# Kernel optimization log

Hardware: AMD Instinct MI355X
Metric: run time of the kernel (lower is better)

## Reference

```python
import jax, jax.numpy as jnp
import numpy as np

INPUT_DIM = 512
NUM_CLASSES = 1000


def setup_inputs() -> dict:
    key = jax.random.key(0)
    kx, kw, kb = jax.random.split(key, 3)
    x = jax.random.normal(kx, (16384, INPUT_DIM), dtype=jnp.float32)
    # Stacked per-class Linear(input_dim, 2) params: W [C, 2, D], b [C, 2]
    lim = 1.0 / np.sqrt(INPUT_DIM)
    W = jax.random.uniform(kw, (NUM_CLASSES, 2, INPUT_DIM), dtype=jnp.float32, minval=-lim, maxval=lim)
    b = jax.random.uniform(kb, (NUM_CLASSES, 2), dtype=jnp.float32, minval=-lim, maxval=lim)
    return {"x": x, "W": W, "b": b}


def reference(x, W, b):
    # logits[b, c, t] = x[b, :] @ W[c, t, :] + b[c, t]
    logits = jnp.einsum("bd,ctd->bct", x, W) + b[None, :, :]  # [B, C, 2]
    # LogSoftmax over the 2 logits per class (torch dim=1 of the [B,2] slice)
    return jax.nn.log_softmax(logits, axis=-1)
```

## Files before the change

### kernel.cpp

```cpp
#include <hip/hip_runtime.h>
#include <cstdint>
#include <cstddef>

typedef unsigned short u16;
typedef unsigned int u32;
typedef __bf16 bf16x8 __attribute__((ext_vector_type(8)));
typedef float f32x4 __attribute__((ext_vector_type(4)));
typedef float f32x2 __attribute__((ext_vector_type(2)));
typedef u32 u32x4 __attribute__((ext_vector_type(4)));

#define M_TOT 16384
#define C_TOT 1000
#define N_PAD 1024
#define K_TOT 512
#define OUT_STRIDE 2000
#define BM 128
#define BN 128
#define BK 32
#define NT 16
#define NWG 1024

__device__ __forceinline__ u16 f2bf(float f) {
  u32 u = __float_as_uint(f);
  u = (u + 0x7FFFu + ((u >> 16) & 1u)) >> 16;
  return (u16)u;
}

__device__ __forceinline__ u32 cvtpk(float lo, float hi) {
  u32 d;
  asm("v_cvt_pk_bf16_f32 %0, %1, %2" : "=v"(d) : "v"(lo), "v"(hi));
  return d;
}

__global__ __launch_bounds__(256) void wprep_kernel(const float* __restrict__ W,
                                                    const float* __restrict__ b,
                                                    u16* __restrict__ wd,
                                                    float* __restrict__ bd) {
  const int i = blockIdx.x * 256 + threadIdx.x;
  const int c = i >> 6;
  const int seg = i & 63;
  ushort4 r0 = {0, 0, 0, 0}, r1 = {0, 0, 0, 0};
  if (c < C_TOT) {
    const float4* w0 = (const float4*)(W + (size_t)(2 * c) * K_TOT) + seg * 2;
    const float4* w1 = (const float4*)(W + (size_t)(2 * c + 1) * K_TOT) + seg * 2;
    float4 a0 = w0[0], a1 = w0[1], c0 = w1[0], c1 = w1[1];
    r0.x = f2bf(a0.x - c0.x); r0.y = f2bf(a0.y - c0.y);
    r0.z = f2bf(a0.z - c0.z); r0.w = f2bf(a0.w - c0.w);
    r1.x = f2bf(a1.x - c1.x); r1.y = f2bf(a1.y - c1.y);
    r1.z = f2bf(a1.z - c1.z); r1.w = f2bf(a1.w - c1.w);
    if (seg == 0) bd[c] = b[2 * c] - b[2 * c + 1];
  } else if (seg == 0) {
    bd[c] = 0.0f;
  }
  ushort4* d = (ushort4*)(wd + (size_t)c * K_TOT);
  d[seg * 2] = r0;
  d[seg * 2 + 1] = r1;
}

__device__ __forceinline__ void gload_lds(const u16* g, u16* l) {
  __builtin_amdgcn_global_load_lds((const __attribute__((address_space(1))) u32*)g,
                                   (__attribute__((address_space(3))) u32*)l, 16, 0, 0);
}

__device__ __forceinline__ void stage8k(const u16* __restrict__ gbase,
                                        u16* lb, int tid) {
#pragma unroll
  for (int i = 0; i < 2; ++i) {
    const int g = i * 256 + tid;
    const int lrow = g >> 3;
    const int u = (g & 7) ^ (lrow & 7);
    const int r = lrow | ((u >> 2) << 6);
    const int q = u & 3;
    gload_lds(gbase + (size_t)r * K_TOT + q * 8, lb + (size_t)g * 8);
  }
}

#define VMW(N) asm volatile("s_waitcnt vmcnt(" #N ")" ::: "memory")
#define CFENCE asm volatile("" ::: "memory")

__global__ __launch_bounds__(256, 2) void gemm_ls_kernel(const float* __restrict__ Af,
                                                         const u16* __restrict__ B,
                                                         const float* __restrict__ bdiff,
                                                         float* __restrict__ out) {
  __shared__ u16 As[4][4096];
  __shared__ u16 Bs[4][4096];

  const int tid = threadIdx.x;
  const int lane = tid & 63;
  const int w = tid >> 6;
  const int wm = w >> 1;
  const int wn = w & 1;

  const int bid = blockIdx.x;
  const int wg = (bid & 7) * (NWG / 8) + (bid >> 3);
  const int m0 = (wg >> 3) * BM;
  const int n0 = (wg & 7) * BN;

  const float* gAf = Af + (size_t)m0 * K_TOT;
  const u16* gB = B + (size_t)n0 * K_TOT;

  const int lrow0 = tid >> 3;
  const int au = (tid & 7) ^ (lrow0 & 7);
  const int qA = au & 3;
  const int rA0 = lrow0 | ((au >> 2) << 6);
  const int rA1 = (32 + lrow0) | ((au >> 2) << 6);
  const f32x4* gq0 = (const f32x4*)gAf + (size_t)rA0 * 128 + qA * 2;
  const f32x4* gq1 = (const f32x4*)gAf + (size_t)rA1 * 128 + qA * 2;

  const int ar = lane & 15;
  const int kq4 = lane >> 4;
  int offA[4], offB[4];
#pragma unroll
  for (int i = 0; i < 4; ++i) {
    int r = wm * 64 + i * 16 + ar;
    offA[i] = (r & 63) * 128 + (((((r >> 6) << 2) | kq4) ^ (r & 7)) << 4);
    r = wn * 64 + i * 16 + ar;
    offB[i] = (r & 63) * 128 + (((((r >> 6) << 2) | kq4) ^ (r & 7)) << 4);
  }

  f32x4 acc[4][4] = {};
  f32x4 areg[3][4];

#define ALOAD(T)                                   \
  do {                                             \
    areg[(T) % 3][0] = gq0[(T) * 8];               \
    areg[(T) % 3][1] = gq0[(T) * 8 + 1];           \
    areg[(T) % 3][2] = gq1[(T) * 8];               \
    areg[(T) % 3][3] = gq1[(T) * 8 + 1];           \
  } while (0)

#define ACVT_WR(T)                                                        \
  do {                                                                    \
    u32x4 w0, w1;                                                         \
    w0.x = cvtpk(areg[(T) % 3][0].x, areg[(T) % 3][0].y);                 \
    w0.y = cvtpk(areg[(T) % 3][0].z, areg[(T) % 3][0].w);                 \
    w0.z = cvtpk(areg[(T) % 3][1].x, areg[(T) % 3][1].y);                 \
    w0.w = cvtpk(areg[(T) % 3][1].z, areg[(T) % 3][1].w);                 \
    w1.x = cvtpk(areg[(T) % 3][2].x, areg[(T) % 3][2].y);                 \
    w1.y = cvtpk(areg[(T) % 3][2].z, areg[(T) % 3][2].w);                 \
    w1.z = cvtpk(areg[(T) % 3][3].x, areg[(T) % 3][3].y);                 \
    w1.w = cvtpk(areg[(T) % 3][3].z, areg[(T) % 3][3].w);                 \
    *(u32x4*)(&As[(T) & 3][(size_t)tid * 8]) = w0;                        \
    *(u32x4*)(&As[(T) & 3][(size_t)(256 + tid) * 8]) = w1;                \
  } while (0)

#define BSTAGE(T) stage8k(gB + (T) * BK, &Bs[(T) & 3][0], tid)

#define COMPUTE(T)                                                          \
  do {                                                                      \
    bf16x8 af[4], bf[4];                                                    \
    _Pragma("unroll") for (int i = 0; i < 4; ++i)                           \
        af[i] = *(const bf16x8*)((const char*)&As[(T) & 3][0] + offA[i]);   \
    _Pragma("unroll") for (int i = 0; i < 4; ++i)                           \
        bf[i] = *(const bf16x8*)((const char*)&Bs[(T) & 3][0] + offB[i]);   \
    _Pragma("unroll") for (int mi = 0; mi < 4; ++mi)                        \
        _Pragma("unroll") for (int ni = 0; ni < 4; ++ni)                    \
            acc[mi][ni] = __builtin_amdgcn_mfma_f32_16x16x32_bf16(          \
                af[mi], bf[ni], acc[mi][ni], 0, 0, 0);                      \
  } while (0)

#define STEP(T, VMN)                                         \
  do {                                                       \
    VMW(VMN);                                                \
    CFENCE;                                                  \
    ACVT_WR(T);                                              \
    if ((T) + 3 < NT) ALOAD((T) + 3);                        \
    asm volatile("s_waitcnt lgkmcnt(0)" ::: "memory");       \
    __builtin_amdgcn_s_barrier();                            \
    CFENCE;                                                  \
    if ((T) + 3 < NT) BSTAGE((T) + 3);                       \
    __builtin_amdgcn_s_setprio(1);                           \
    COMPUTE(T);                                              \
    __builtin_amdgcn_s_setprio(0);                           \
  } while (0)

  ALOAD(0); BSTAGE(0);
  ALOAD(1); BSTAGE(1);
  ALOAD(2); BSTAGE(2);

  STEP(0, 12);  STEP(1, 12);  STEP(2, 12);  STEP(3, 12);
  STEP(4, 12);  STEP(5, 12);  STEP(6, 12);  STEP(7, 12);
  STEP(8, 12);  STEP(9, 12);  STEP(10, 12); STEP(11, 12);
  STEP(12, 12); STEP(13, 12); STEP(14, 6);  STEP(15, 0);

  const int rbase = m0 + wm * 64 + (lane >> 4) * 4;
  const bool full = (n0 + BN <= C_TOT);

#pragma unroll
  for (int ni = 0; ni < 4; ++ni) {
    const int n = n0 + wn * 64 + ni * 16 + ar;
    if (full || n < C_TOT) {
      const float bd_r = bdiff[n];
#pragma unroll
      for (int mi = 0; mi < 4; ++mi) {
#pragma unroll
        for (int j = 0; j < 4; ++j) {
          const float d = acc[mi][ni][j] + bd_r;
          const float o0 = fminf(d, 0.0f) - __logf(1.0f + __expf(-fabsf(d)));
          const int row = rbase + mi * 16 + j;
          f32x2 v;
          v.x = o0;
          v.y = o0 - d;
          *(f32x2*)(out + (size_t)row * OUT_STRIDE + 2 * n) = v;
        }
      }
    }
  }
#undef ALOAD
#undef ACVT_WR
#undef BSTAGE
#undef COMPUTE
#undef STEP
}

__global__ __launch_bounds__(256) void naive_kernel(const float* __restrict__ x,
                                                    const float* __restrict__ W,
                                                    const float* __restrict__ b,
                                                    float* __restrict__ out) {
  __shared__ float xs[K_TOT];
  const int row = blockIdx.x;
  for (int i = threadIdx.x; i < K_TOT; i += 256) xs[i] = x[(size_t)row * K_TOT + i];
  __syncthreads();
  for (int c = threadIdx.x; c < C_TOT; c += 256) {
    const float* w0 = W + (size_t)c * 1024;
    float l0 = b[c * 2], l1 = b[c * 2 + 1];
    for (int k = 0; k < K_TOT; ++k) {
      const float xv = xs[k];
      l0 += xv * w0[k];
      l1 += xv * w0[K_TOT + k];
    }
    const float d = l0 - l1;
    const float t = __logf(1.0f + __expf(-fabsf(d)));
    out[(size_t)row * OUT_STRIDE + c * 2]     = fminf(d, 0.0f) - t;
    out[(size_t)row * OUT_STRIDE + c * 2 + 1] = fminf(-d, 0.0f) - t;
  }
}

extern "C" void kernel_launch(void* const* d_in, const int* in_sizes, int n_in,
                              void* d_out, int out_size, void* d_ws, size_t ws_size,
                              hipStream_t stream) {
  const float* x = (const float*)d_in[0];
  const float* W = (const float*)d_in[1];
  const float* b = (const float*)d_in[2];
  float* out = (float*)d_out;

  const size_t nwd = (size_t)N_PAD * K_TOT;
  const size_t need = nwd * sizeof(u16) + N_PAD * sizeof(float);

  if (ws_size < need) {
    naive_kernel<<<M_TOT, 256, 0, stream>>>(x, W, b, out);
    return;
  }

  u16* wd = (u16*)d_ws;
  float* bd = (float*)(wd + nwd);

  wprep_kernel<<<256, 256, 0, stream>>>(W, b, wd, bd);
  gemm_ls_kernel<<<NWG, 256, 0, stream>>>(x, wd, bd, out);
}
```

Measured before the change: 50.91 us.

## Shallow the load pipeline to fit four workgroups per CU

Reduces the software pipeline depth: A is now prefetched one step ahead into double-buffered LDS and registers, and B two steps ahead into a triple LDS buffer. LDS and register use shrink, so launch bounds rise to four workgroups per CU. The idea is to hide memory latency through more resident waves instead of deep per-wave prefetch. The shallower prefetch exposes more latency per wave, and the vmcnt wait counts were retuned to match.

```diff
diff --git a/kernel.cpp b/kernel.cpp
--- a/kernel.cpp
+++ b/kernel.cpp
@@ -78,12 +78,12 @@
 #define VMW(N) asm volatile("s_waitcnt vmcnt(" #N ")" ::: "memory")
 #define CFENCE asm volatile("" ::: "memory")
 
-__global__ __launch_bounds__(256, 2) void gemm_ls_kernel(const float* __restrict__ Af,
+__global__ __launch_bounds__(256, 4) void gemm_ls_kernel(const float* __restrict__ Af,
                                                          const u16* __restrict__ B,
                                                          const float* __restrict__ bdiff,
                                                          float* __restrict__ out) {
-  __shared__ u16 As[4][4096];
-  __shared__ u16 Bs[4][4096];
+  __shared__ u16 As[2][4096];
+  __shared__ u16 Bs[3][4096];
 
   const int tid = threadIdx.x;
   const int lane = tid & 63;
@@ -119,40 +119,40 @@
   }
 
   f32x4 acc[4][4] = {};
-  f32x4 areg[3][4];
+  f32x4 areg[2][4];
 
 #define ALOAD(T)                                   \
   do {                                             \
-    areg[(T) % 3][0] = gq0[(T) * 8];               \
-    areg[(T) % 3][1] = gq0[(T) * 8 + 1];           \
-    areg[(T) % 3][2] = gq1[(T) * 8];               \
-    areg[(T) % 3][3] = gq1[(T) * 8 + 1];           \
+    areg[(T) & 1][0] = gq0[(T) * 8];               \
+    areg[(T) & 1][1] = gq0[(T) * 8 + 1];           \
+    areg[(T) & 1][2] = gq1[(T) * 8];               \
+    areg[(T) & 1][3] = gq1[(T) * 8 + 1];           \
   } while (0)
 
 #define ACVT_WR(T)                                                        \
   do {                                                                    \
     u32x4 w0, w1;                                                         \
-    w0.x = cvtpk(areg[(T) % 3][0].x, areg[(T) % 3][0].y);                 \
-    w0.y = cvtpk(areg[(T) % 3][0].z, areg[(T) % 3][0].w);                 \
-    w0.z = cvtpk(areg[(T) % 3][1].x, areg[(T) % 3][1].y);                 \
-    w0.w = cvtpk(areg[(T) % 3][1].z, areg[(T) % 3][1].w);                 \
-    w1.x = cvtpk(areg[(T) % 3][2].x, areg[(T) % 3][2].y);                 \
-    w1.y = cvtpk(areg[(T) % 3][2].z, areg[(T) % 3][2].w);                 \
-    w1.z = cvtpk(areg[(T) % 3][3].x, areg[(T) % 3][3].y);                 \
-    w1.w = cvtpk(areg[(T) % 3][3].z, areg[(T) % 3][3].w);                 \
-    *(u32x4*)(&As[(T) & 3][(size_t)tid * 8]) = w0;                        \
-    *(u32x4*)(&As[(T) & 3][(size_t)(256 + tid) * 8]) = w1;                \
-  } while (0)
-
-#define BSTAGE(T) stage8k(gB + (T) * BK, &Bs[(T) & 3][0], tid)
+    w0.x = cvtpk(areg[(T) & 1][0].x, areg[(T) & 1][0].y);                 \
+    w0.y = cvtpk(areg[(T) & 1][0].z, areg[(T) & 1][0].w);                 \
+    w0.z = cvtpk(areg[(T) & 1][1].x, areg[(T) & 1][1].y);                 \
+    w0.w = cvtpk(areg[(T) & 1][1].z, areg[(T) & 1][1].w);                 \
+    w1.x = cvtpk(areg[(T) & 1][2].x, areg[(T) & 1][2].y);                 \
+    w1.y = cvtpk(areg[(T) & 1][2].z, areg[(T) & 1][2].w);                 \
+    w1.z = cvtpk(areg[(T) & 1][3].x, areg[(T) & 1][3].y);                 \
+    w1.w = cvtpk(areg[(T) & 1][3].z, areg[(T) & 1][3].w);                 \
+    *(u32x4*)(&As[(T) & 1][(size_t)tid * 8]) = w0;                        \
+    *(u32x4*)(&As[(T) & 1][(size_t)(256 + tid) * 8]) = w1;                \
+  } while (0)
+
+#define BSTAGE(T) stage8k(gB + (T) * BK, &Bs[(T) % 3][0], tid)
 
 #define COMPUTE(T)                                                          \
   do {                                                                      \
     bf16x8 af[4], bf[4];                                                    \
     _Pragma("unroll") for (int i = 0; i < 4; ++i)                           \
-        af[i] = *(const bf16x8*)((const char*)&As[(T) & 3][0] + offA[i]);   \
+        af[i] = *(const bf16x8*)((const char*)&As[(T) & 1][0] + offA[i]);   \
     _Pragma("unroll") for (int i = 0; i < 4; ++i)                           \
-        bf[i] = *(const bf16x8*)((const char*)&Bs[(T) & 3][0] + offB[i]);   \
+        bf[i] = *(const bf16x8*)((const char*)&Bs[(T) % 3][0] + offB[i]);   \
     _Pragma("unroll") for (int mi = 0; mi < 4; ++mi)                        \
         _Pragma("unroll") for (int ni = 0; ni < 4; ++ni)                    \
             acc[mi][ni] = __builtin_amdgcn_mfma_f32_16x16x32_bf16(          \
@@ -164,24 +164,26 @@
     VMW(VMN);                                                \
     CFENCE;                                                  \
     ACVT_WR(T);                                              \
-    if ((T) + 3 < NT) ALOAD((T) + 3);                        \
+    if ((T) + 1 < NT) ALOAD((T) + 1);                        \
     asm volatile("s_waitcnt lgkmcnt(0)" ::: "memory");       \
     __builtin_amdgcn_s_barrier();                            \
     CFENCE;                                                  \
-    if ((T) + 3 < NT) BSTAGE((T) + 3);                       \
+    if ((T) + 2 < NT) BSTAGE((T) + 2);                       \
     __builtin_amdgcn_s_setprio(1);                           \
     COMPUTE(T);                                              \
     __builtin_amdgcn_s_setprio(0);                           \
   } while (0)
 
-  ALOAD(0); BSTAGE(0);
-  ALOAD(1); BSTAGE(1);
-  ALOAD(2); BSTAGE(2);
-
-  STEP(0, 12);  STEP(1, 12);  STEP(2, 12);  STEP(3, 12);
-  STEP(4, 12);  STEP(5, 12);  STEP(6, 12);  STEP(7, 12);
-  STEP(8, 12);  STEP(9, 12);  STEP(10, 12); STEP(11, 12);
-  STEP(12, 12); STEP(13, 12); STEP(14, 6);  STEP(15, 0);
+  ALOAD(0);
+  CFENCE;
+  BSTAGE(0);
+  BSTAGE(1);
+  CFENCE;
+
+  STEP(0, 2);   STEP(1, 2);   STEP(2, 2);   STEP(3, 2);
+  STEP(4, 2);   STEP(5, 2);   STEP(6, 2);   STEP(7, 2);
+  STEP(8, 2);   STEP(9, 2);   STEP(10, 2);  STEP(11, 2);
+  STEP(12, 2);  STEP(13, 2);  STEP(14, 2);  STEP(15, 0);
 
   const int rbase = m0 + wm * 64 + (lane >> 4) * 4;
   const bool full = (n0 + BN <= C_TOT);
```

Result: faster. 48.78 us, median of 4 (-4.2%).
